# Kernel tuning notes

Hardware: AMD Instinct MI355X
Metric: run time of the kernel (lower is better)

Reference implementation:

```python
import jax, jax.numpy as jnp
import numpy as np

N, A, C = 524288, 256, 19
IGNORE = 255


def setup_inputs() -> dict:
    key = jax.random.key(0)
    k1, k2, k3, k4, k5 = jax.random.split(key, 5)
    features = jax.random.normal(k1, (N, A), dtype=jnp.float32)
    labels = jax.random.randint(k2, (N,), 0, C, dtype=jnp.int64)
    Mean = jax.random.normal(k3, (C, A), dtype=jnp.float32)
    CoVariance = jax.random.uniform(k4, (C, A), dtype=jnp.float32)
    Amount = jax.random.uniform(k5, (C,), dtype=jnp.float32)
    return {"features": features, "labels": labels, "Mean": Mean,
            "CoVariance": CoVariance, "Amount": Amount}


def reference(features, labels, Mean, CoVariance, Amount):
    C_, A_ = Mean.shape
    mask = (labels != IGNORE)
    safe = jnp.where(mask, labels, 0)            # masked rows routed to class 0 with zero weight
    fmask = mask.astype(features.dtype)[:, None]
    # per-class counts and sums (replaces the O(N*C*A) onehot blowup)
    count = jax.ops.segment_sum(fmask[:, 0], safe, num_segments=C_)        # [C]
    count_c = jnp.maximum(count, 1.0)                                      # Amount_CxA[==0]=1
    mean = jax.ops.segment_sum(features * fmask, safe, num_segments=C_) / count_c[:, None]  # [C,A]
    diff = (features - mean[safe]) * fmask
    var = jax.ops.segment_sum(diff * diff, safe, num_segments=C_) / count_c[:, None]        # [C,A]
    # EMA-style merge with running stats
    w = count[:, None] / (count[:, None] + Amount[:, None])
    w = jnp.where(jnp.isnan(w), 0.0, w)          # weight_CV[weight_CV != weight_CV] = 0
    additional_CV = w * (1.0 - w) * jnp.square(Mean - mean)
    new_CoV = CoVariance * (1.0 - w) + var * w + additional_CV
    new_Mean = Mean * (1.0 - w) + mean * w
    new_Amount = Amount + count
    # pack outputs: [C, A] | [C, A] | [C, 1] -> [C, 2A+1]
    return jnp.concatenate([new_CoV, new_Mean, new_Amount[:, None]], axis=1)
```

## Files before the change

kernel.cpp:

```cpp
#include <hip/hip_runtime.h>

#define NROW 524288
#define NA 256
#define NC 19
#define IGN 255
#define SQOFF  (NC * NA)
#define CNTOFF (2 * NC * NA)
#define NCELL  (2 * NC * NA + NC)
#define OUTSTRIDE (2 * NA + 1)

__global__ __launch_bounds__(256, 4) void k_accum(
    const float* __restrict__ feat, const int* __restrict__ lab,
    float* __restrict__ part, int rpb)
{
    __shared__ float acc[NCELL];
    const int t = threadIdx.x;
    for (int i = t; i < NCELL; i += 256) acc[i] = 0.0f;
    __syncthreads();

    const int r0 = blockIdx.x * rpb;
    const int r1 = min(r0 + rpb, NROW);

    for (int r = r0 + t; r < r1; r += 256) {
        int c = lab[r];
        if (c != IGN) atomicAdd(&acc[CNTOFF + c], 1.0f);
    }

    const float* fp = feat + (size_t)r0 * NA + t;
    #pragma unroll 8
    for (int r = r0; r < r1; ++r, fp += NA) {
        int c = lab[r];
        float x = *fp;
        if (c != IGN) {
            int base = c * NA + t;
            acc[base] += x;
            acc[SQOFF + base] += x * x;
        }
    }
    __syncthreads();

    float* dst = part + (size_t)blockIdx.x * NCELL;
    for (int i = t; i < NCELL; i += 256) dst[i] = acc[i];
}

__global__ void k_reduce(const float* __restrict__ part, float* __restrict__ part2,
                         int nb, int bper)
{
    int col = blockIdx.x * 256 + threadIdx.x;
    if (col >= NCELL) return;
    int b0 = blockIdx.y * bper;
    int b1 = min(b0 + bper, nb);
    float s = 0.0f;
    const float* p = part + (size_t)b0 * NCELL + col;
    for (int b = b0; b < b1; ++b, p += NCELL) s += *p;
    part2[(size_t)blockIdx.y * NCELL + col] = s;
}

__global__ void k_final(const float* __restrict__ part2, int nr,
                        const float* __restrict__ Mean, const float* __restrict__ CoV,
                        const float* __restrict__ Amt, float* __restrict__ out)
{
    int c = blockIdx.x;
    int a = threadIdx.x;
    float s = 0.0f, q = 0.0f, cnt = 0.0f;
    for (int i = 0; i < nr; ++i) {
        const float* p = part2 + (size_t)i * NCELL;
        s   += p[c * NA + a];
        q   += p[SQOFF + c * NA + a];
        cnt += p[CNTOFF + c];
    }
    float amt  = Amt[c];
    float cc   = fmaxf(cnt, 1.0f);
    float mean = s / cc;
    float var  = 0.0f;
    if (cnt > 0.0f) {
        double dv = ((double)q - (double)s * (double)s / (double)cnt) / (double)cnt;
        var = (float)(dv > 0.0 ? dv : 0.0);
    }
    float denom = cnt + amt;
    float w  = (denom != 0.0f) ? (cnt / denom) : 0.0f;
    float om = 1.0f - w;
    float mu0 = Mean[c * NA + a];
    float cv0 = CoV[c * NA + a];
    float d   = mu0 - mean;
    float ncv = cv0 * om + var * w + w * om * d * d;
    float nmu = mu0 * om + mean * w;
    out[c * OUTSTRIDE + a]      = ncv;
    out[c * OUTSTRIDE + NA + a] = nmu;
    if (a == 0) out[c * OUTSTRIDE + 2 * NA] = amt + cnt;
}

extern "C" void kernel_launch(void* const* d_in, const int* in_sizes, int n_in,
                              void* d_out, int out_size, void* d_ws, size_t ws_size,
                              hipStream_t stream)
{
    const float* feat = (const float*)d_in[0];
    const int*   lab  = (const int*)d_in[1];
    const float* Mean = (const float*)d_in[2];
    const float* CoV  = (const float*)d_in[3];
    const float* Amt  = (const float*)d_in[4];
    float* out = (float*)d_out;

    const size_t bufBytes = (size_t)NCELL * sizeof(float);
    size_t cap = ws_size / bufBytes;
    int B = 1024, R = 8;
    if (cap < (size_t)(B + R)) {
        if (cap >= 16) { R = 8; B = (int)cap - R; }
        else if (cap >= 2) { R = 1; B = (int)cap - 1; }
        else { R = 1; B = 1; }
    }
    if (R > B) R = B;

    float* part  = (float*)d_ws;
    float* part2 = part + (size_t)B * NCELL;
    int rpb  = (NROW + B - 1) / B;
    int bper = (B + R - 1) / R;

    hipLaunchKernelGGL(k_accum, dim3(B), dim3(256), 0, stream,
                       feat, lab, part, rpb);
    hipLaunchKernelGGL(k_reduce, dim3((NCELL + 255) / 256, R), dim3(256), 0, stream,
                       part, part2, B, bper);
    hipLaunchKernelGGL(k_final, dim3(NC), dim3(256), 0, stream,
                       part2, R, Mean, CoV, Amt, out);
}
```

Measured before the change: 885.0 us.

## Process four rows per block step with float4 loads and shared atomics

The accumulation kernel now assigns each of the four wavefronts its own row, and each lane loads a float4. Because different waves can hit the same class, the sums go through shared-memory atomics, which replaces the serial per-row loop that had one float per thread. The shared accumulator layout is reordered by component, class and lane, and the final kernel's indexing is updated to match. The change gives wider loads and more rows in flight at the cost of eight LDS atomics per lane per row, plus float atomic contention and nondeterministic summation order.

```diff
diff --git a/kernel.cpp b/kernel.cpp
--- a/kernel.cpp
+++ b/kernel.cpp
@@ -4,9 +4,9 @@
 #define NA 256
 #define NC 19
 #define IGN 255
-#define SQOFF  (NC * NA)
-#define CNTOFF (2 * NC * NA)
-#define NCELL  (2 * NC * NA + NC)
+#define SQOFF  (4 * NC * 64)
+#define CNTOFF (2 * SQOFF)
+#define NCELL  (2 * SQOFF + NC)
 #define OUTSTRIDE (2 * NA + 1)
 
 __global__ __launch_bounds__(256, 4) void k_accum(
@@ -15,26 +15,56 @@
 {
     __shared__ float acc[NCELL];
     const int t = threadIdx.x;
+    const int wave = t >> 6, lane = t & 63;
     for (int i = t; i < NCELL; i += 256) acc[i] = 0.0f;
     __syncthreads();
 
     const int r0 = blockIdx.x * rpb;
     const int r1 = min(r0 + rpb, NROW);
+    const int nrows = r1 - r0;
+    const float4* __restrict__ fg = (const float4*)feat;
 
-    for (int r = r0 + t; r < r1; r += 256) {
-        int c = lab[r];
-        if (c != IGN) atomicAdd(&acc[CNTOFF + c], 1.0f);
-    }
-
-    const float* fp = feat + (size_t)r0 * NA + t;
-    #pragma unroll 8
-    for (int r = r0; r < r1; ++r, fp += NA) {
-        int c = lab[r];
-        float x = *fp;
-        if (c != IGN) {
-            int base = c * NA + t;
-            acc[base] += x;
-            acc[SQOFF + base] += x * x;
+    if ((nrows & 3) == 0 && nrows > 0) {
+        const int ngrp = nrows >> 2;
+        const float4* p = fg + (size_t)(r0 + wave) * 64 + lane;
+        const int* lp = lab + r0 + wave;
+        #pragma unroll 8
+        for (int g = 0; g < ngrp; ++g, p += 256, lp += 4) {
+            int c = *lp;
+            float4 v = *p;
+            if ((unsigned)c < NC) {
+                int b0 = c * 64 + lane;
+                atomicAdd(&acc[b0],                 v.x);
+                atomicAdd(&acc[b0 + SQOFF],         v.x * v.x);
+                atomicAdd(&acc[b0 + NC * 64],       v.y);
+                atomicAdd(&acc[b0 + NC * 64 + SQOFF], v.y * v.y);
+                atomicAdd(&acc[b0 + 2 * NC * 64],   v.z);
+                atomicAdd(&acc[b0 + 2 * NC * 64 + SQOFF], v.z * v.z);
+                atomicAdd(&acc[b0 + 3 * NC * 64],   v.w);
+                atomicAdd(&acc[b0 + 3 * NC * 64 + SQOFF], v.w * v.w);
+                if (lane == 0) atomicAdd(&acc[CNTOFF + c], 1.0f);
+            }
+        }
+    } else {
+        const int ngrp = (nrows + 3) >> 2;
+        for (int g = 0; g < ngrp; ++g) {
+            int r = r0 + g * 4 + wave;
+            if (r < r1) {
+                int c = lab[r];
+                float4 v = fg[(size_t)r * 64 + lane];
+                if ((unsigned)c < NC) {
+                    int b0 = c * 64 + lane;
+                    atomicAdd(&acc[b0],                 v.x);
+                    atomicAdd(&acc[b0 + SQOFF],         v.x * v.x);
+                    atomicAdd(&acc[b0 + NC * 64],       v.y);
+                    atomicAdd(&acc[b0 + NC * 64 + SQOFF], v.y * v.y);
+                    atomicAdd(&acc[b0 + 2 * NC * 64],   v.z);
+                    atomicAdd(&acc[b0 + 2 * NC * 64 + SQOFF], v.z * v.z);
+                    atomicAdd(&acc[b0 + 3 * NC * 64],   v.w);
+                    atomicAdd(&acc[b0 + 3 * NC * 64 + SQOFF], v.w * v.w);
+                    if (lane == 0) atomicAdd(&acc[CNTOFF + c], 1.0f);
+                }
+            }
         }
     }
     __syncthreads();
@@ -62,11 +92,13 @@
 {
     int c = blockIdx.x;
     int a = threadIdx.x;
+    int j = a & 3, l = a >> 2;
+    int idx = (j * NC + c) * 64 + l;
     float s = 0.0f, q = 0.0f, cnt = 0.0f;
     for (int i = 0; i < nr; ++i) {
         const float* p = part2 + (size_t)i * NCELL;
-        s   += p[c * NA + a];
-        q   += p[SQOFF + c * NA + a];
+        s   += p[idx];
+        q   += p[idx + SQOFF];
         cnt += p[CNTOFF + c];
     }
     float amt  = Amt[c];
```

Result: slower. 1.921 ms (+117.1%).

## Accumulate per-class sums in registers with wave-uniform switch, float2 loads

Applied to the files above, without the earlier changes.

Replaces the shared-memory read-modify-write accumulation in k_accum with per-thread register accumulators for all 19 classes. Each wave picks its class through a wave-uniform switch on readfirstlane of the label, and loads features as float2. Two wave-rows each take alternate rows and are merged through shared memory at the end. Counts are now kept in integer registers instead of LDS atomics. This removes LDS traffic and the separate label pass, at the cost of heavy register use (lower occupancy hint, 3) and a branchy switch per row.

```diff
diff --git a/kernel.cpp b/kernel.cpp
--- a/kernel.cpp
+++ b/kernel.cpp
@@ -9,38 +9,81 @@
 #define NCELL  (2 * NC * NA + NC)
 #define OUTSTRIDE (2 * NA + 1)
 
-__global__ __launch_bounds__(256, 4) void k_accum(
+__global__ __launch_bounds__(256, 3) void k_accum(
     const float* __restrict__ feat, const int* __restrict__ lab,
     float* __restrict__ part, int rpb)
 {
-    __shared__ float acc[NCELL];
+    __shared__ float red[NCELL];
     const int t = threadIdx.x;
-    for (int i = t; i < NCELL; i += 256) acc[i] = 0.0f;
-    __syncthreads();
+    const int w = t >> 6, lane = t & 63;
+    const int half = w & 1;
+    const int wr = w >> 1;
+    const int col0 = half * 128 + lane * 2;
+
+    float2 s[NC], q[NC];
+    #pragma unroll
+    for (int k = 0; k < NC; ++k) {
+        s[k] = make_float2(0.f, 0.f);
+        q[k] = make_float2(0.f, 0.f);
+    }
+    int cnt[NC];
+    #pragma unroll
+    for (int k = 0; k < NC; ++k) cnt[k] = 0;
+    const int inc = (half == 0) ? 1 : 0;
 
     const int r0 = blockIdx.x * rpb;
     const int r1 = min(r0 + rpb, NROW);
+    const float2* __restrict__ fg = (const float2*)feat;
 
-    for (int r = r0 + t; r < r1; r += 256) {
-        int c = lab[r];
-        if (c != IGN) atomicAdd(&acc[CNTOFF + c], 1.0f);
+    #pragma unroll 4
+    for (int r = r0 + wr; r < r1; r += 2) {
+        int c = __builtin_amdgcn_readfirstlane(lab[r]);
+        float2 v = fg[(size_t)r * 128 + half * 64 + lane];
+        switch (c) {
+#define CASE_K(k) case k: \
+            s[k].x += v.x; s[k].y += v.y; \
+            q[k].x += v.x * v.x; q[k].y += v.y * v.y; \
+            cnt[k] += inc; break;
+            CASE_K(0)  CASE_K(1)  CASE_K(2)  CASE_K(3)  CASE_K(4)
+            CASE_K(5)  CASE_K(6)  CASE_K(7)  CASE_K(8)  CASE_K(9)
+            CASE_K(10) CASE_K(11) CASE_K(12) CASE_K(13) CASE_K(14)
+            CASE_K(15) CASE_K(16) CASE_K(17) CASE_K(18)
+#undef CASE_K
+            default: break;
+        }
     }
 
-    const float* fp = feat + (size_t)r0 * NA + t;
-    #pragma unroll 8
-    for (int r = r0; r < r1; ++r, fp += NA) {
-        int c = lab[r];
-        float x = *fp;
-        if (c != IGN) {
-            int base = c * NA + t;
-            acc[base] += x;
-            acc[SQOFF + base] += x * x;
+    if (wr == 0) {
+        #pragma unroll
+        for (int k = 0; k < NC; ++k) {
+            *(float2*)&red[k * NA + col0]         = s[k];
+            *(float2*)&red[SQOFF + k * NA + col0] = q[k];
+        }
+        if (lane == 0 && half == 0) {
+            #pragma unroll
+            for (int k = 0; k < NC; ++k) red[CNTOFF + k] = (float)cnt[k];
+        }
+    }
+    __syncthreads();
+    if (wr == 1) {
+        #pragma unroll
+        for (int k = 0; k < NC; ++k) {
+            float2 a = *(float2*)&red[k * NA + col0];
+            a.x += s[k].x; a.y += s[k].y;
+            *(float2*)&red[k * NA + col0] = a;
+            float2 b = *(float2*)&red[SQOFF + k * NA + col0];
+            b.x += q[k].x; b.y += q[k].y;
+            *(float2*)&red[SQOFF + k * NA + col0] = b;
+        }
+        if (lane == 0 && half == 0) {
+            #pragma unroll
+            for (int k = 0; k < NC; ++k) red[CNTOFF + k] += (float)cnt[k];
         }
     }
     __syncthreads();
 
     float* dst = part + (size_t)blockIdx.x * NCELL;
-    for (int i = t; i < NCELL; i += 256) dst[i] = acc[i];
+    for (int i = t; i < NCELL; i += 256) dst[i] = red[i];
 }
 
 __global__ void k_reduce(const float* __restrict__ part, float* __restrict__ part2,
@@ -50,10 +93,10 @@
     if (col >= NCELL) return;
     int b0 = blockIdx.y * bper;
     int b1 = min(b0 + bper, nb);
-    float s = 0.0f;
+    float sum = 0.0f;
     const float* p = part + (size_t)b0 * NCELL + col;
-    for (int b = b0; b < b1; ++b, p += NCELL) s += *p;
-    part2[(size_t)blockIdx.y * NCELL + col] = s;
+    for (int b = b0; b < b1; ++b, p += NCELL) sum += *p;
+    part2[(size_t)blockIdx.y * NCELL + col] = sum;
 }
 
 __global__ void k_final(const float* __restrict__ part2, int nr,
@@ -62,11 +105,12 @@
 {
     int c = blockIdx.x;
     int a = threadIdx.x;
+    int idx = c * NA + a;
     float s = 0.0f, q = 0.0f, cnt = 0.0f;
     for (int i = 0; i < nr; ++i) {
         const float* p = part2 + (size_t)i * NCELL;
-        s   += p[c * NA + a];
-        q   += p[SQOFF + c * NA + a];
+        s   += p[idx];
+        q   += p[idx + SQOFF];
         cnt += p[CNTOFF + c];
     }
     float amt  = Amt[c];
@@ -80,8 +124,8 @@
     float denom = cnt + amt;
     float w  = (denom != 0.0f) ? (cnt / denom) : 0.0f;
     float om = 1.0f - w;
-    float mu0 = Mean[c * NA + a];
-    float cv0 = CoV[c * NA + a];
+    float mu0 = Mean[idx];
+    float cv0 = CoV[idx];
     float d   = mu0 - mean;
     float ncv = cv0 * om + var * w + w * om * d * d;
     float nmu = mu0 * om + mean * w;
```

After: 3.333 ms. +276.6%, slower.

## Accumulate per-class sums in registers using wave ballots instead of LDS

Applied to the files above, without the earlier changes.

The accumulation kernel now keeps per-class sum and sum-of-squares in registers as float2 for all 19 classes. It walks each 64-row batch class by class, using ballot masks to visit only the rows that carry that label. Two wave groups split the rows, each half covering 128 columns, and their results are merged through LDS at the end. This removes the per-row LDS read-modify-write and the LDS atomic count, and it widens feature loads to float2. In exchange it raises register pressure (occupancy hint drops from 4 to 3), adds serial ballot loops per class, and makes the row-gathered loads less regular.

```diff
diff --git a/kernel.cpp b/kernel.cpp
--- a/kernel.cpp
+++ b/kernel.cpp
@@ -9,38 +9,90 @@
 #define NCELL  (2 * NC * NA + NC)
 #define OUTSTRIDE (2 * NA + 1)
 
-__global__ __launch_bounds__(256, 4) void k_accum(
+#define DECL_K(k) float2 s##k = make_float2(0.f,0.f), q##k = make_float2(0.f,0.f); int n##k = 0;
+#define ACC_K(k, v) { s##k.x += (v).x; s##k.y += (v).y; \
+                      q##k.x += (v).x*(v).x; q##k.y += (v).y*(v).y; }
+#define KCLS(k) { \
+    unsigned long long m = __ballot(lc == (k)); \
+    n##k += (int)__popcll(m); \
+    if (m) { \
+        int b = (int)__builtin_ctzll(m); m &= m - 1ull; \
+        float2 v = fb[(size_t)b * 128]; \
+        while (m) { \
+            int b2 = (int)__builtin_ctzll(m); m &= m - 1ull; \
+            float2 vn = fb[(size_t)b2 * 128];    \
+            ACC_K(k, v); \
+            v = vn; \
+        } \
+        ACC_K(k, v); \
+    } }
+
+__global__ __launch_bounds__(256, 3) void k_accum(
     const float* __restrict__ feat, const int* __restrict__ lab,
     float* __restrict__ part, int rpb)
 {
-    __shared__ float acc[NCELL];
+    __shared__ float red[2 * NC * NA];
+    __shared__ float wc[2][NC];
     const int t = threadIdx.x;
-    for (int i = t; i < NCELL; i += 256) acc[i] = 0.0f;
-    __syncthreads();
+    const int wave = t >> 6, lane = t & 63;
+    const int half = wave & 1;
+    const int grp  = wave >> 1;
+
+    DECL_K(0)  DECL_K(1)  DECL_K(2)  DECL_K(3)  DECL_K(4)
+    DECL_K(5)  DECL_K(6)  DECL_K(7)  DECL_K(8)  DECL_K(9)
+    DECL_K(10) DECL_K(11) DECL_K(12) DECL_K(13) DECL_K(14)
+    DECL_K(15) DECL_K(16) DECL_K(17) DECL_K(18)
 
     const int r0 = blockIdx.x * rpb;
     const int r1 = min(r0 + rpb, NROW);
+    const int nbatch = (r1 - r0 + 63) >> 6;
+    const float2* __restrict__ feat2 = (const float2*)feat;
 
-    for (int r = r0 + t; r < r1; r += 256) {
-        int c = lab[r];
-        if (c != IGN) atomicAdd(&acc[CNTOFF + c], 1.0f);
+    for (int g = grp; g < nbatch; g += 2) {
+        const int rb = r0 + g * 64;
+        const int rown = rb + lane;
+        const int lc = (rown < r1) ? lab[rown] : -1;
+        const float2* fb = feat2 + (size_t)rb * 128 + half * 64 + lane;
+        KCLS(0)  KCLS(1)  KCLS(2)  KCLS(3)  KCLS(4)
+        KCLS(5)  KCLS(6)  KCLS(7)  KCLS(8)  KCLS(9)
+        KCLS(10) KCLS(11) KCLS(12) KCLS(13) KCLS(14)
+        KCLS(15) KCLS(16) KCLS(17) KCLS(18)
     }
 
-    const float* fp = feat + (size_t)r0 * NA + t;
-    #pragma unroll 8
-    for (int r = r0; r < r1; ++r, fp += NA) {
-        int c = lab[r];
-        float x = *fp;
-        if (c != IGN) {
-            int base = c * NA + t;
-            acc[base] += x;
-            acc[SQOFF + base] += x * x;
-        }
+    const int col0 = half * 128 + lane * 2;
+#define WR_K(k) { *(float2*)&red[(k) * NA + col0] = s##k; \
+                  *(float2*)&red[SQOFF + (k) * NA + col0] = q##k; }
+#define ADD_K(k) { float2 a = *(float2*)&red[(k) * NA + col0]; \
+                   a.x += s##k.x; a.y += s##k.y; \
+                   *(float2*)&red[(k) * NA + col0] = a; \
+                   float2 b = *(float2*)&red[SQOFF + (k) * NA + col0]; \
+                   b.x += q##k.x; b.y += q##k.y; \
+                   *(float2*)&red[SQOFF + (k) * NA + col0] = b; }
+#define WC_K(k) wc[grp][k] = (float)n##k;
+    if (grp == 0) {
+        WR_K(0)  WR_K(1)  WR_K(2)  WR_K(3)  WR_K(4)
+        WR_K(5)  WR_K(6)  WR_K(7)  WR_K(8)  WR_K(9)
+        WR_K(10) WR_K(11) WR_K(12) WR_K(13) WR_K(14)
+        WR_K(15) WR_K(16) WR_K(17) WR_K(18)
+    }
+    if (half == 0 && lane == 0) {
+        WC_K(0)  WC_K(1)  WC_K(2)  WC_K(3)  WC_K(4)
+        WC_K(5)  WC_K(6)  WC_K(7)  WC_K(8)  WC_K(9)
+        WC_K(10) WC_K(11) WC_K(12) WC_K(13) WC_K(14)
+        WC_K(15) WC_K(16) WC_K(17) WC_K(18)
+    }
+    __syncthreads();
+    if (grp == 1) {
+        ADD_K(0)  ADD_K(1)  ADD_K(2)  ADD_K(3)  ADD_K(4)
+        ADD_K(5)  ADD_K(6)  ADD_K(7)  ADD_K(8)  ADD_K(9)
+        ADD_K(10) ADD_K(11) ADD_K(12) ADD_K(13) ADD_K(14)
+        ADD_K(15) ADD_K(16) ADD_K(17) ADD_K(18)
     }
     __syncthreads();
 
     float* dst = part + (size_t)blockIdx.x * NCELL;
-    for (int i = t; i < NCELL; i += 256) dst[i] = acc[i];
+    for (int i = t; i < 2 * NC * NA; i += 256) dst[i] = red[i];
+    if (t < NC) dst[CNTOFF + t] = wc[0][t] + wc[1][t];
 }
 
 __global__ void k_reduce(const float* __restrict__ part, float* __restrict__ part2,
@@ -50,10 +102,10 @@
     if (col >= NCELL) return;
     int b0 = blockIdx.y * bper;
     int b1 = min(b0 + bper, nb);
-    float s = 0.0f;
+    float sum = 0.0f;
     const float* p = part + (size_t)b0 * NCELL + col;
-    for (int b = b0; b < b1; ++b, p += NCELL) s += *p;
-    part2[(size_t)blockIdx.y * NCELL + col] = s;
+    for (int b = b0; b < b1; ++b, p += NCELL) sum += *p;
+    part2[(size_t)blockIdx.y * NCELL + col] = sum;
 }
 
 __global__ void k_final(const float* __restrict__ part2, int nr,
@@ -62,11 +114,12 @@
 {
     int c = blockIdx.x;
     int a = threadIdx.x;
+    int idx = c * NA + a;
     float s = 0.0f, q = 0.0f, cnt = 0.0f;
     for (int i = 0; i < nr; ++i) {
         const float* p = part2 + (size_t)i * NCELL;
-        s   += p[c * NA + a];
-        q   += p[SQOFF + c * NA + a];
+        s   += p[idx];
+        q   += p[idx + SQOFF];
         cnt += p[CNTOFF + c];
     }
     float amt  = Amt[c];
@@ -80,8 +133,8 @@
     float denom = cnt + amt;
     float w  = (denom != 0.0f) ? (cnt / denom) : 0.0f;
     float om = 1.0f - w;
-    float mu0 = Mean[c * NA + a];
-    float cv0 = CoV[c * NA + a];
+    float mu0 = Mean[idx];
+    float cv0 = CoV[idx];
     float d   = mu0 - mean;
     float ncv = cv0 * om + var * w + w * om * d * d;
     float nmu = mu0 * om + mean * w;
```

After: 758.5 us. 1.17x faster.
